# Kernel optimization log

Hardware: AMD Instinct MI355X
Metric: run time of the kernel (lower is better)

Reference implementation:

```python
import jax, jax.numpy as jnp
import numpy as np

N = 100000
E = 1600000
DIMS = [256, 192, 128, 64, 3]  # in_features=256, hidden_layer_count=4, last layer -> 3


def setup_inputs() -> dict:
    key = jax.random.key(0)
    ks = jax.random.split(key, 2 + 4 * len(DIMS))
    features = jax.random.normal(ks[0], (N, 256), dtype=jnp.float32)
    # (torch.unique-based normalization implicitly assumes this)
    src = jnp.arange(E, dtype=jnp.int64) % N
    dst = jax.random.randint(ks[1], (E,), 0, N, dtype=jnp.int64)
    edges = jnp.stack([src, dst], axis=1)
    inp = {"features": features, "edges": edges}
    ki = 2
    for li in range(4):
        din, dout = DIMS[li], DIMS[li + 1]
        s = 1.0 / np.sqrt(din)
        inp[f"W0_{li}"] = jax.random.uniform(ks[ki], (din, dout), jnp.float32, -s, s); ki += 1
        inp[f"b0_{li}"] = jax.random.uniform(ks[ki], (dout,), jnp.float32, -s, s); ki += 1
        inp[f"W1_{li}"] = jax.random.uniform(ks[ki], (din, dout), jnp.float32, -s, s); ki += 1
        inp[f"b1_{li}"] = jax.random.uniform(ks[ki], (dout,), jnp.float32, -s, s); ki += 1
    return inp


def _graph_conv_norm(x, edges, deg_inv, W0, b0, W1, b1):
    # pytorch3d GraphConv (undirected): w0(x) + scatter-add of w1(x[neighbor]) over both edge directions,
    # then degree normalization (GraphConvNorm)
    h0 = x @ W0 + b0                       # [N, dout]
    h1 = x @ W1 + b1                       # [N, dout]
    agg = jnp.zeros_like(h0)
    agg = agg.at[edges[:, 0]].add(h1[edges[:, 1]])
    agg = agg.at[edges[:, 1]].add(h1[edges[:, 0]])
    return deg_inv * (h0 + agg)


def reference(features, edges, W0_0, b0_0, W1_0, b1_0, W0_1, b0_1, W1_1, b1_1,
              W0_2, b0_2, W1_2, b1_2, W0_3, b0_3, W1_3, b1_3):
    # degree = occurrence count of each vertex id in edges (== torch.unique(..., return_counts=True)[1])
    deg = jnp.zeros((N,), jnp.float32).at[edges.reshape(-1)].add(1.0)
    deg_inv = (1.0 / deg)[:, None]
    params = [(W0_0, b0_0, W1_0, b1_0), (W0_1, b0_1, W1_1, b1_1), (W0_2, b0_2, W1_2, b1_2)]
    x = features
    for (W0, b0, W1, b1) in params:
        x = jax.nn.relu(_graph_conv_norm(x, edges, deg_inv, W0, b0, W1, b1))
    return _graph_conv_norm(x, edges, deg_inv, W0_3, b0_3, W1_3, b1_3)
```

## Files before the change

### kernel.cpp

```cpp
#include <hip/hip_runtime.h>
#include <hip/hip_fp16.h>

#define NV 100000
#define NE 1600000

#define BM 64
#define BN 64
#define BK 16

#define TBM 128
#define TBN 64
#define TBK 32
#define APAD 40
#define BPAD 40

#define SCAN_B 1024
#define NBLK ((NV + SCAN_B - 1) / SCAN_B)

typedef __attribute__((ext_vector_type(8))) _Float16 f16x8;
typedef __attribute__((ext_vector_type(4))) _Float16 f16x4;
typedef __attribute__((ext_vector_type(4))) float f32x4;

__global__ void degree_count(const int* __restrict__ ef, int* __restrict__ deg, int n) {
    int i = blockIdx.x * blockDim.x + threadIdx.x;
    if (i < n) atomicAdd(&deg[ef[i]], 1);
}

__global__ __launch_bounds__(SCAN_B) void scan_block(const int* __restrict__ deg,
                                                     int* __restrict__ part,
                                                     int* __restrict__ bsum, int n) {
    __shared__ int tmp[SCAN_B];
    const int tid = threadIdx.x;
    const int gid = blockIdx.x * SCAN_B + tid;
    int v = (gid < n) ? deg[gid] : 0;
    tmp[tid] = v;
    __syncthreads();
    for (int off = 1; off < SCAN_B; off <<= 1) {
        int t = (tid >= off) ? tmp[tid - off] : 0;
        __syncthreads();
        tmp[tid] += t;
        __syncthreads();
    }
    if (gid < n) part[gid] = tmp[tid] - v;
    if (tid == SCAN_B - 1) bsum[blockIdx.x] = tmp[tid];
}

__global__ __launch_bounds__(128) void scan_top(int* __restrict__ bsum, int nb) {
    __shared__ int tmp[128];
    const int tid = threadIdx.x;
    int v = (tid < nb) ? bsum[tid] : 0;
    tmp[tid] = v;
    __syncthreads();
    for (int off = 1; off < 128; off <<= 1) {
        int t = (tid >= off) ? tmp[tid - off] : 0;
        __syncthreads();
        tmp[tid] += t;
        __syncthreads();
    }
    if (tid < nb) bsum[tid] = tmp[tid] - v;
}

__global__ __launch_bounds__(SCAN_B) void finalize_rowptr(int* __restrict__ rowptr,
                                                          const int* __restrict__ bsum,
                                                          const int* __restrict__ deg,
                                                          int* __restrict__ fill,
                                                          float* __restrict__ dinv, int n) {
    const int gid = blockIdx.x * SCAN_B + threadIdx.x;
    if (gid < n) {
        int r = rowptr[gid] + bsum[blockIdx.x];
        rowptr[gid] = r;
        fill[gid] = r;
        dinv[gid] = 1.0f / (float)deg[gid];
    }
    if (gid == 0) rowptr[n] = 2 * NE;
}

__global__ void fill_adj(const int* __restrict__ edges, int* __restrict__ fill,
                         int* __restrict__ adj, int nE) {
    int e = blockIdx.x * blockDim.x + threadIdx.x;
    if (e >= nE) return;
    const int a = edges[2 * e];
    const int b = edges[2 * e + 1];
    int pa = atomicAdd(&fill[a], 1); adj[pa] = b;
    int pb = atomicAdd(&fill[b], 1); adj[pb] = a;
}

__global__ __launch_bounds__(256) void gemm_dual_mfma(
    const float* __restrict__ X,
    const float* __restrict__ W0, const float* __restrict__ b0,
    const float* __restrict__ W1, const float* __restrict__ b1,
    float* __restrict__ C0, _Float16* __restrict__ C1,
    int M, int din, int dout)
{
    __shared__ _Float16 As[TBM * APAD];
    __shared__ _Float16 Bs[2][TBN * BPAD];

    const int tid = threadIdx.x;
    const int bm = blockIdx.x * TBM;
    const int bn = blockIdx.y * TBN;
    const int lane = tid & 63;
    const int wid = tid >> 6;
    const int wm = wid >> 1;
    const int wn = wid & 1;
    const int lr = lane & 15;
    const int lk = lane >> 4;

    f32x4 acc[2][4][2] = {};

    const int bn_n = tid & 63;
    const int bn_kb = (tid >> 6) * 8;

    for (int k0 = 0; k0 < din; k0 += TBK) {
        #pragma unroll
        for (int i = 0; i < 4; ++i) {
            const int idx = tid + i * 256;
            const int row = idx >> 3;
            const int q = idx & 7;
            const int grow = bm + row;
            float4 v = {0.f, 0.f, 0.f, 0.f};
            if (grow < M)
                v = *reinterpret_cast<const float4*>(&X[(size_t)grow * din + k0 + q * 4]);
            f16x4 h = { (_Float16)v.x, (_Float16)v.y, (_Float16)v.z, (_Float16)v.w };
            *reinterpret_cast<f16x4*>(&As[row * APAD + q * 4]) = h;
        }
        {
            const float* pw0 = &W0[(size_t)(k0 + bn_kb) * dout + bn + bn_n];
            const float* pw1 = &W1[(size_t)(k0 + bn_kb) * dout + bn + bn_n];
            _Float16* d0 = &Bs[0][bn_n * BPAD + bn_kb];
            _Float16* d1 = &Bs[1][bn_n * BPAD + bn_kb];
            #pragma unroll
            for (int i = 0; i < 8; ++i) {
                d0[i] = (_Float16)pw0[(size_t)i * dout];
                d1[i] = (_Float16)pw1[(size_t)i * dout];
            }
        }
        __syncthreads();

        f16x8 a[4], b[2][2];
        #pragma unroll
        for (int mf = 0; mf < 4; ++mf)
            a[mf] = *reinterpret_cast<const f16x8*>(&As[(wm * 64 + mf * 16 + lr) * APAD + lk * 8]);
        #pragma unroll
        for (int o = 0; o < 2; ++o)
            #pragma unroll
            for (int nf = 0; nf < 2; ++nf)
                b[o][nf] = *reinterpret_cast<const f16x8*>(&Bs[o][(wn * 32 + nf * 16 + lr) * BPAD + lk * 8]);

        #pragma unroll
        for (int o = 0; o < 2; ++o)
            #pragma unroll
            for (int mf = 0; mf < 4; ++mf)
                #pragma unroll
                for (int nf = 0; nf < 2; ++nf)
                    acc[o][mf][nf] = __builtin_amdgcn_mfma_f32_16x16x32_f16(
                        a[mf], b[o][nf], acc[o][mf][nf], 0, 0, 0);

        __syncthreads();
    }

    #pragma unroll
    for (int mf = 0; mf < 4; ++mf) {
        #pragma unroll
        for (int reg = 0; reg < 4; ++reg) {
            const int row = bm + wm * 64 + mf * 16 + lk * 4 + reg;
            if (row >= M) continue;
            #pragma unroll
            for (int nf = 0; nf < 2; ++nf) {
                const int c = bn + wn * 32 + nf * 16 + lr;
                C0[(size_t)row * dout + c] = acc[0][mf][nf][reg] + b0[c];
                C1[(size_t)row * dout + c] = (_Float16)(acc[1][mf][nf][reg] + b1[c]);
            }
        }
    }
}

__global__ __launch_bounds__(256) void gemm_dual_bias_f32(
    const float* __restrict__ X,
    const float* __restrict__ W0, const float* __restrict__ b0,
    const float* __restrict__ W1, const float* __restrict__ b1,
    float* __restrict__ C0, float* __restrict__ C1,
    int M, int din, int dout)
{
    __shared__ float As[BM][BK + 1];
    __shared__ float Bs0[BK][BN];
    __shared__ float Bs1[BK][BN];

    const int tid = threadIdx.x;
    const int bm = blockIdx.x * BM;
    const int bn = blockIdx.y * BN;
    const int tx = tid & 15;
    const int ty = tid >> 4;

    const int ar = tid >> 2;
    const int ac = (tid & 3) * 4;
    const int br = tid >> 4;
    const int bc = (tid & 15) * 4;

    float acc0[4][4] = {};
    float acc1[4][4] = {};

    for (int k0 = 0; k0 < din; k0 += BK) {
        {
            const int grow = bm + ar;
            if (grow < M) {
                const float4 v = *reinterpret_cast<const float4*>(&X[(size_t)grow * din + k0 + ac]);
                As[ar][ac + 0] = v.x; As[ar][ac + 1] = v.y;
                As[ar][ac + 2] = v.z; As[ar][ac + 3] = v.w;
            } else {
                As[ar][ac + 0] = 0.f; As[ar][ac + 1] = 0.f;
                As[ar][ac + 2] = 0.f; As[ar][ac + 3] = 0.f;
            }
        }
        {
            const int gk = k0 + br;
            const int gc = bn + bc;
            float4 v0, v1;
            v0.x = (gc + 0 < dout) ? W0[(size_t)gk * dout + gc + 0] : 0.f;
            v0.y = (gc + 1 < dout) ? W0[(size_t)gk * dout + gc + 1] : 0.f;
            v0.z = (gc + 2 < dout) ? W0[(size_t)gk * dout + gc + 2] : 0.f;
            v0.w = (gc + 3 < dout) ? W0[(size_t)gk * dout + gc + 3] : 0.f;
            v1.x = (gc + 0 < dout) ? W1[(size_t)gk * dout + gc + 0] : 0.f;
            v1.y = (gc + 1 < dout) ? W1[(size_t)gk * dout + gc + 1] : 0.f;
            v1.z = (gc + 2 < dout) ? W1[(size_t)gk * dout + gc + 2] : 0.f;
            v1.w = (gc + 3 < dout) ? W1[(size_t)gk * dout + gc + 3] : 0.f;
            *reinterpret_cast<float4*>(&Bs0[br][bc]) = v0;
            *reinterpret_cast<float4*>(&Bs1[br][bc]) = v1;
        }
        __syncthreads();

        #pragma unroll
        for (int kk = 0; kk < BK; ++kk) {
            const float a0 = As[ty * 4 + 0][kk];
            const float a1 = As[ty * 4 + 1][kk];
            const float a2 = As[ty * 4 + 2][kk];
            const float a3 = As[ty * 4 + 3][kk];
            const float4 p = *reinterpret_cast<const float4*>(&Bs0[kk][tx * 4]);
            const float4 q = *reinterpret_cast<const float4*>(&Bs1[kk][tx * 4]);
            acc0[0][0] += a0 * p.x; acc0[0][1] += a0 * p.y; acc0[0][2] += a0 * p.z; acc0[0][3] += a0 * p.w;
            acc0[1][0] += a1 * p.x; acc0[1][1] += a1 * p.y; acc0[1][2] += a1 * p.z; acc0[1][3] += a1 * p.w;
            acc0[2][0] += a2 * p.x; acc0[2][1] += a2 * p.y; acc0[2][2] += a2 * p.z; acc0[2][3] += a2 * p.w;
            acc0[3][0] += a3 * p.x; acc0[3][1] += a3 * p.y; acc0[3][2] += a3 * p.z; acc0[3][3] += a3 * p.w;
            acc1[0][0] += a0 * q.x; acc1[0][1] += a0 * q.y; acc1[0][2] += a0 * q.z; acc1[0][3] += a0 * q.w;
            acc1[1][0] += a1 * q.x; acc1[1][1] += a1 * q.y; acc1[1][2] += a1 * q.z; acc1[1][3] += a1 * q.w;
            acc1[2][0] += a2 * q.x; acc1[2][1] += a2 * q.y; acc1[2][2] += a2 * q.z; acc1[2][3] += a2 * q.w;
            acc1[3][0] += a3 * q.x; acc1[3][1] += a3 * q.y; acc1[3][2] += a3 * q.z; acc1[3][3] += a3 * q.w;
        }
        __syncthreads();
    }

    #pragma unroll
    for (int i = 0; i < 4; ++i) {
        const int row = bm + ty * 4 + i;
        if (row >= M) continue;
        #pragma unroll
        for (int j = 0; j < 4; ++j) {
            const int col = bn + tx * 4 + j;
            if (col < dout) {
                C0[(size_t)row * dout + col] = acc0[i][j] + b0[col];
                C1[(size_t)row * dout + col] = acc1[i][j] + b1[col];
            }
        }
    }
}

__global__ __launch_bounds__(256) void gather_d192_h(
    const float* __restrict__ h0, const __half2* __restrict__ h1,
    const int* __restrict__ rowptr, const int* __restrict__ adj,
    const float* __restrict__ dinv, float* __restrict__ out)
{
    const int v = blockIdx.x * 4 + (threadIdx.x >> 6);
    if (v >= NV) return;
    const int lane = threadIdx.x & 63;
    const int sub = lane >> 5;
    const int cu = (lane & 31) * 3;
    const int s = rowptr[v], e = rowptr[v + 1];

    float2 a0 = {0.f, 0.f}, a1 = {0.f, 0.f}, a2 = {0.f, 0.f};

    int j = s;
    const int jend = s + ((e - s) & ~3);
    for (; j < jend; j += 4) {
        const __half2* r0 = h1 + (size_t)adj[j + sub] * 96 + cu;
        const __half2* r1 = h1 + (size_t)adj[j + 2 + sub] * 96 + cu;
        const float2 p0 = __half22float2(r0[0]);
        const float2 p1 = __half22float2(r0[1]);
        const float2 p2 = __half22float2(r0[2]);
        const float2 q0 = __half22float2(r1[0]);
        const float2 q1 = __half22float2(r1[1]);
        const float2 q2 = __half22float2(r1[2]);
        a0.x += p0.x + q0.x; a0.y += p0.y + q0.y;
        a1.x += p1.x + q1.x; a1.y += p1.y + q1.y;
        a2.x += p2.x + q2.x; a2.y += p2.y + q2.y;
    }
    for (; j < e; j += 2) {
        const int jj = j + sub;
        if (jj < e) {
            const __half2* r = h1 + (size_t)adj[jj] * 96 + cu;
            const float2 p0 = __half22float2(r[0]);
            const float2 p1 = __half22float2(r[1]);
            const float2 p2 = __half22float2(r[2]);
            a0.x += p0.x; a0.y += p0.y;
            a1.x += p1.x; a1.y += p1.y;
            a2.x += p2.x; a2.y += p2.y;
        }
    }

    a0.x += __shfl_xor(a0.x, 32); a0.y += __shfl_xor(a0.y, 32);
    a1.x += __shfl_xor(a1.x, 32); a1.y += __shfl_xor(a1.y, 32);
    a2.x += __shfl_xor(a2.x, 32); a2.y += __shfl_xor(a2.y, 32);

    if (sub == 0) {
        const float di = dinv[v];
        const size_t base = (size_t)v * 192 + (size_t)cu * 2;
        float2 o0, o1, o2;
        o0.x = fmaxf((h0[base + 0] + a0.x) * di, 0.f);
        o0.y = fmaxf((h0[base + 1] + a0.y) * di, 0.f);
        o1.x = fmaxf((h0[base + 2] + a1.x) * di, 0.f);
        o1.y = fmaxf((h0[base + 3] + a1.y) * di, 0.f);
        o2.x = fmaxf((h0[base + 4] + a2.x) * di, 0.f);
        o2.y = fmaxf((h0[base + 5] + a2.y) * di, 0.f);
        *reinterpret_cast<float2*>(out + base + 0) = o0;
        *reinterpret_cast<float2*>(out + base + 2) = o1;
        *reinterpret_cast<float2*>(out + base + 4) = o2;
    }
}

__global__ __launch_bounds__(256) void gather_d128_h(
    const float* __restrict__ h0, const __half2* __restrict__ h1,
    const int* __restrict__ rowptr, const int* __restrict__ adj,
    const float* __restrict__ dinv, float* __restrict__ out)
{
    const int v = blockIdx.x * 4 + (threadIdx.x >> 6);
    if (v >= NV) return;
    const int lane = threadIdx.x & 63;
    const int sub = lane >> 4;
    const int cu = (lane & 15) * 4;
    const int s = rowptr[v], e = rowptr[v + 1];

    float acc[8] = {};

    int j = s;
    const int jend = s + ((e - s) & ~7);
    for (; j < jend; j += 8) {
        const int4 w0 = *reinterpret_cast<const int4*>(h1 + (size_t)adj[j + sub] * 64 + cu);
        const int4 w1 = *reinterpret_cast<const int4*>(h1 + (size_t)adj[j + 4 + sub] * 64 + cu);
        #pragma unroll
        for (int t = 0; t < 4; ++t) {
            const float2 p = __half22float2(*(const __half2*)(&(&w0.x)[t]));
            const float2 q = __half22float2(*(const __half2*)(&(&w1.x)[t]));
            acc[2 * t + 0] += p.x + q.x;
            acc[2 * t + 1] += p.y + q.y;
        }
    }
    for (; j < e; j += 4) {
        const int jj = j + sub;
        if (jj < e) {
            const int4 w0 = *reinterpret_cast<const int4*>(h1 + (size_t)adj[jj] * 64 + cu);
            #pragma unroll
            for (int t = 0; t < 4; ++t) {
                const float2 p = __half22float2(*(const __half2*)(&(&w0.x)[t]));
                acc[2 * t + 0] += p.x;
                acc[2 * t + 1] += p.y;
            }
        }
    }

    #pragma unroll
    for (int t = 0; t < 8; ++t) {
        acc[t] += __shfl_xor(acc[t], 16);
        acc[t] += __shfl_xor(acc[t], 32);
    }

    if (sub == 0) {
        const float di = dinv[v];
        const size_t base = (size_t)v * 128 + (size_t)cu * 2;
        float4 o0, o1;
        o0.x = fmaxf((h0[base + 0] + acc[0]) * di, 0.f);
        o0.y = fmaxf((h0[base + 1] + acc[1]) * di, 0.f);
        o0.z = fmaxf((h0[base + 2] + acc[2]) * di, 0.f);
        o0.w = fmaxf((h0[base + 3] + acc[3]) * di, 0.f);
        o1.x = fmaxf((h0[base + 4] + acc[4]) * di, 0.f);
        o1.y = fmaxf((h0[base + 5] + acc[5]) * di, 0.f);
        o1.z = fmaxf((h0[base + 6] + acc[6]) * di, 0.f);
        o1.w = fmaxf((h0[base + 7] + acc[7]) * di, 0.f);
        *reinterpret_cast<float4*>(out + base + 0) = o0;
        *reinterpret_cast<float4*>(out + base + 4) = o1;
    }
}

__global__ __launch_bounds__(256) void gather_d64_h(
    const float* __restrict__ h0, const __half2* __restrict__ h1,
    const int* __restrict__ rowptr, const int* __restrict__ adj,
    const float* __restrict__ dinv, float* __restrict__ out)
{
    const int v = blockIdx.x * 4 + (threadIdx.x >> 6);
    if (v >= NV) return;
    const int lane = threadIdx.x & 63;
    const int sub = lane >> 3;
    const int cu = (lane & 7) * 4;
    const int s = rowptr[v], e = rowptr[v + 1];

    float acc[8] = {};

    int j = s;
    const int jend = s + ((e - s) & ~15);
    for (; j < jend; j += 16) {
        const int4 w0 = *reinterpret_cast<const int4*>(h1 + (size_t)adj[j + sub] * 32 + cu);
        const int4 w1 = *reinterpret_cast<const int4*>(h1 + (size_t)adj[j + 8 + sub] * 32 + cu);
        #pragma unroll
        for (int t = 0; t < 4; ++t) {
            const float2 p = __half22float2(*(const __half2*)(&(&w0.x)[t]));
            const float2 q = __half22float2(*(const __half2*)(&(&w1.x)[t]));
            acc[2 * t + 0] += p.x + q.x;
            acc[2 * t + 1] += p.y + q.y;
        }
    }
    for (; j < e; j += 8) {
        const int jj = j + sub;
        if (jj < e) {
            const int4 w0 = *reinterpret_cast<const int4*>(h1 + (size_t)adj[jj] * 32 + cu);
            #pragma unroll
            for (int t = 0; t < 4; ++t) {
                const float2 p = __half22float2(*(const __half2*)(&(&w0.x)[t]));
                acc[2 * t + 0] += p.x;
                acc[2 * t + 1] += p.y;
            }
        }
    }

    #pragma unroll
    for (int t = 0; t < 8; ++t) {
        acc[t] += __shfl_xor(acc[t], 8);
        acc[t] += __shfl_xor(acc[t], 16);
        acc[t] += __shfl_xor(acc[t], 32);
    }

    if (sub == 0) {
        const float di = dinv[v];
        const size_t base = (size_t)v * 64 + (size_t)cu * 2;
        float4 o0, o1;
        o0.x = fmaxf((h0[base + 0] + acc[0]) * di, 0.f);
        o0.y = fmaxf((h0[base + 1] + acc[1]) * di, 0.f);
        o0.z = fmaxf((h0[base + 2] + acc[2]) * di, 0.f);
        o0.w = fmaxf((h0[base + 3] + acc[3]) * di, 0.f);
        o1.x = fmaxf((h0[base + 4] + acc[4]) * di, 0.f);
        o1.y = fmaxf((h0[base + 5] + acc[5]) * di, 0.f);
        o1.z = fmaxf((h0[base + 6] + acc[6]) * di, 0.f);
        o1.w = fmaxf((h0[base + 7] + acc[7]) * di, 0.f);
        *reinterpret_cast<float4*>(out + base + 0) = o0;
        *reinterpret_cast<float4*>(out + base + 4) = o1;
    }
}

__global__ __launch_bounds__(256) void gather_d3(
    const float* __restrict__ h0, const float* __restrict__ h1,
    const int* __restrict__ rowptr, const int* __restrict__ adj,
    const float* __restrict__ dinv, float* __restrict__ out)
{
    const int v = blockIdx.x * 4 + (threadIdx.x >> 6);
    if (v >= NV) return;
    const int lane = threadIdx.x & 63;
    const int s = rowptr[v], e = rowptr[v + 1];
    float a0 = 0.f, a1 = 0.f, a2 = 0.f;
    for (int j = s + lane; j < e; j += 64) {
        const float3 r = *reinterpret_cast<const float3*>(h1 + (size_t)adj[j] * 3);
        a0 += r.x; a1 += r.y; a2 += r.z;
    }
    #pragma unroll
    for (int off = 1; off < 64; off <<= 1) {
        a0 += __shfl_xor(a0, off);
        a1 += __shfl_xor(a1, off);
        a2 += __shfl_xor(a2, off);
    }
    if (lane == 0) {
        const float di = dinv[v];
        const size_t base = (size_t)v * 3;
        out[base + 0] = (h0[base + 0] + a0) * di;
        out[base + 1] = (h0[base + 1] + a1) * di;
        out[base + 2] = (h0[base + 2] + a2) * di;
    }
}

extern "C" void kernel_launch(void* const* d_in, const int* in_sizes, int n_in,
                              void* d_out, int out_size, void* d_ws, size_t ws_size,
                              hipStream_t stream) {
    const float* features = (const float*)d_in[0];
    const int*   edges    = (const int*)d_in[1];

    char* ws = (char*)d_ws;
    size_t off = 0;
    auto alloc = [&](size_t bytes) {
        void* p = ws + off;
        off = (off + bytes + 255) & ~(size_t)255;
        return p;
    };
    int*   deg    = (int*)alloc((size_t)NV * sizeof(int));
    float* dinv   = (float*)alloc((size_t)NV * sizeof(float));
    int*   rowptr = (int*)alloc((size_t)(NV + 1) * sizeof(int));
    int*   fill   = (int*)alloc((size_t)NV * sizeof(int));
    int*   bsum   = (int*)alloc(256 * sizeof(int));
    int*   adj    = (int*)alloc((size_t)2 * NE * sizeof(int));
    float* buf0   = (float*)alloc((size_t)NV * 192 * sizeof(float));
    void*  buf1   = alloc((size_t)NV * 192 * sizeof(float));
    float* buf2   = (float*)alloc((size_t)NV * 128 * sizeof(float));

    hipMemsetAsync(deg, 0, (size_t)NV * sizeof(int), stream);
    degree_count<<<(2 * NE + 255) / 256, 256, 0, stream>>>(edges, deg, 2 * NE);
    scan_block<<<NBLK, SCAN_B, 0, stream>>>(deg, rowptr, bsum, NV);
    scan_top<<<1, 128, 0, stream>>>(bsum, NBLK);
    finalize_rowptr<<<NBLK, SCAN_B, 0, stream>>>(rowptr, bsum, deg, fill, dinv, NV);
    fill_adj<<<(NE + 255) / 256, 256, 0, stream>>>(edges, fill, adj, NE);

    const int dims[5] = {256, 192, 128, 64, 3};
    const float* Xp[4];
    float* C0p[4];
    Xp[0] = features; C0p[0] = buf0;
    Xp[1] = buf0;     C0p[1] = buf2;
    Xp[2] = buf2;     C0p[2] = buf0;
    Xp[3] = buf0;     C0p[3] = buf2;

    const int gatherGrid = (NV + 3) / 4;

    for (int li = 0; li < 4; ++li) {
        const int din  = dims[li];
        const int dout = dims[li + 1];
        const float* W0 = (const float*)d_in[2 + li * 4 + 0];
        const float* b0 = (const float*)d_in[2 + li * 4 + 1];
        const float* W1 = (const float*)d_in[2 + li * 4 + 2];
        const float* b1 = (const float*)d_in[2 + li * 4 + 3];

        if (li < 3) {
            dim3 grid((NV + TBM - 1) / TBM, dout / TBN);
            gemm_dual_mfma<<<grid, 256, 0, stream>>>(Xp[li], W0, b0, W1, b1,
                                                     C0p[li], (_Float16*)buf1, NV, din, dout);
        } else {
            dim3 grid((NV + BM - 1) / BM, (dout + BN - 1) / BN);
            gemm_dual_bias_f32<<<grid, 256, 0, stream>>>(Xp[li], W0, b0, W1, b1,
                                                         C0p[li], (float*)buf1, NV, din, dout);
        }

        float* dst = (li < 3) ? C0p[li] : (float*)d_out;
        if (li == 0)
            gather_d192_h<<<gatherGrid, 256, 0, stream>>>(C0p[li], (const __half2*)buf1,
                                                          rowptr, adj, dinv, dst);
        else if (li == 1)
            gather_d128_h<<<gatherGrid, 256, 0, stream>>>(C0p[li], (const __half2*)buf1,
                                                          rowptr, adj, dinv, dst);
        else if (li == 2)
            gather_d64_h<<<gatherGrid, 256, 0, stream>>>(C0p[li], (const __half2*)buf1,
                                                         rowptr, adj, dinv, dst);
        else
            gather_d3<<<gatherGrid, 256, 0, stream>>>(C0p[li], (const float*)buf1,
                                                      rowptr, adj, dinv, dst);
    }
}
```

Before: 806.5 us.

## Store inter-layer activations in fp16 and widen gather unrolling

The gather kernels now write ReLU activations as fp16 instead of fp32, and the following GEMMs read fp16 input directly through a templated load path. This halves activation write and read traffic between layers. The neighbor loops in the gather kernels are also unrolled to four rows per iteration for more memory-level parallelism, and the d64 gather is remapped to 16 lanes of 2 half2 each. The cost is reduced precision in the stored activations.

```diff
diff --git a/kernel.cpp b/kernel.cpp
--- a/kernel.cpp
+++ b/kernel.cpp
@@ -19,6 +19,7 @@
 
 typedef __attribute__((ext_vector_type(8))) _Float16 f16x8;
 typedef __attribute__((ext_vector_type(4))) _Float16 f16x4;
+typedef __attribute__((ext_vector_type(2))) _Float16 f16x2;
 typedef __attribute__((ext_vector_type(4))) float f32x4;
 
 __global__ void degree_count(const int* __restrict__ ef, int* __restrict__ deg, int n) {
@@ -85,8 +86,9 @@
     int pb = atomicAdd(&fill[b], 1); adj[pb] = a;
 }
 
+template <typename XT>
 __global__ __launch_bounds__(256) void gemm_dual_mfma(
-    const float* __restrict__ X,
+    const XT* __restrict__ X,
     const float* __restrict__ W0, const float* __restrict__ b0,
     const float* __restrict__ W1, const float* __restrict__ b1,
     float* __restrict__ C0, _Float16* __restrict__ C1,
@@ -111,17 +113,31 @@
     const int bn_kb = (tid >> 6) * 8;
 
     for (int k0 = 0; k0 < din; k0 += TBK) {
-        #pragma unroll
-        for (int i = 0; i < 4; ++i) {
-            const int idx = tid + i * 256;
-            const int row = idx >> 3;
-            const int q = idx & 7;
-            const int grow = bm + row;
-            float4 v = {0.f, 0.f, 0.f, 0.f};
-            if (grow < M)
-                v = *reinterpret_cast<const float4*>(&X[(size_t)grow * din + k0 + q * 4]);
-            f16x4 h = { (_Float16)v.x, (_Float16)v.y, (_Float16)v.z, (_Float16)v.w };
-            *reinterpret_cast<f16x4*>(&As[row * APAD + q * 4]) = h;
+        if constexpr (sizeof(XT) == 4) {
+            #pragma unroll
+            for (int i = 0; i < 4; ++i) {
+                const int idx = tid + i * 256;
+                const int row = idx >> 3;
+                const int q = idx & 7;
+                const int grow = bm + row;
+                float4 v = {0.f, 0.f, 0.f, 0.f};
+                if (grow < M)
+                    v = *reinterpret_cast<const float4*>(&X[(size_t)grow * din + k0 + q * 4]);
+                f16x4 h = { (_Float16)v.x, (_Float16)v.y, (_Float16)v.z, (_Float16)v.w };
+                *reinterpret_cast<f16x4*>(&As[row * APAD + q * 4]) = h;
+            }
+        } else {
+            #pragma unroll
+            for (int i = 0; i < 2; ++i) {
+                const int idx = tid + i * 256;
+                const int row = idx >> 2;
+                const int q = idx & 3;
+                const int grow = bm + row;
+                f16x8 h = {};
+                if (grow < M)
+                    h = *reinterpret_cast<const f16x8*>(&X[(size_t)grow * din + k0 + q * 8]);
+                *reinterpret_cast<f16x8*>(&As[row * APAD + q * 8]) = h;
+            }
         }
         {
             const float* pw0 = &W0[(size_t)(k0 + bn_kb) * dout + bn + bn_n];
@@ -175,7 +191,7 @@
 }
 
 __global__ __launch_bounds__(256) void gemm_dual_bias_f32(
-    const float* __restrict__ X,
+    const _Float16* __restrict__ X,
     const float* __restrict__ W0, const float* __restrict__ b0,
     const float* __restrict__ W1, const float* __restrict__ b1,
     float* __restrict__ C0, float* __restrict__ C1,
@@ -203,9 +219,9 @@
         {
             const int grow = bm + ar;
             if (grow < M) {
-                const float4 v = *reinterpret_cast<const float4*>(&X[(size_t)grow * din + k0 + ac]);
-                As[ar][ac + 0] = v.x; As[ar][ac + 1] = v.y;
-                As[ar][ac + 2] = v.z; As[ar][ac + 3] = v.w;
+                const f16x4 v = *reinterpret_cast<const f16x4*>(&X[(size_t)grow * din + k0 + ac]);
+                As[ar][ac + 0] = (float)v[0]; As[ar][ac + 1] = (float)v[1];
+                As[ar][ac + 2] = (float)v[2]; As[ar][ac + 3] = (float)v[3];
             } else {
                 As[ar][ac + 0] = 0.f; As[ar][ac + 1] = 0.f;
                 As[ar][ac + 2] = 0.f; As[ar][ac + 3] = 0.f;
@@ -266,7 +282,7 @@
 __global__ __launch_bounds__(256) void gather_d192_h(
     const float* __restrict__ h0, const __half2* __restrict__ h1,
     const int* __restrict__ rowptr, const int* __restrict__ adj,
-    const float* __restrict__ dinv, float* __restrict__ out)
+    const float* __restrict__ dinv, _Float16* __restrict__ out)
 {
     const int v = blockIdx.x * 4 + (threadIdx.x >> 6);
     if (v >= NV) return;
@@ -278,30 +294,42 @@
     float2 a0 = {0.f, 0.f}, a1 = {0.f, 0.f}, a2 = {0.f, 0.f};
 
     int j = s;
-    const int jend = s + ((e - s) & ~3);
-    for (; j < jend; j += 4) {
-        const __half2* r0 = h1 + (size_t)adj[j + sub] * 96 + cu;
-        const __half2* r1 = h1 + (size_t)adj[j + 2 + sub] * 96 + cu;
-        const float2 p0 = __half22float2(r0[0]);
-        const float2 p1 = __half22float2(r0[1]);
-        const float2 p2 = __half22float2(r0[2]);
-        const float2 q0 = __half22float2(r1[0]);
-        const float2 q1 = __half22float2(r1[1]);
-        const float2 q2 = __half22float2(r1[2]);
-        a0.x += p0.x + q0.x; a0.y += p0.y + q0.y;
-        a1.x += p1.x + q1.x; a1.y += p1.y + q1.y;
-        a2.x += p2.x + q2.x; a2.y += p2.y + q2.y;
+    const int jend = s + ((e - s) & ~7);
+    for (; j < jend; j += 8) {
+        const int u0 = adj[j + 0 + sub];
+        const int u1 = adj[j + 2 + sub];
+        const int u2 = adj[j + 4 + sub];
+        const int u3 = adj[j + 6 + sub];
+        const __half2* r0 = h1 + (size_t)u0 * 96 + cu;
+        const __half2* r1 = h1 + (size_t)u1 * 96 + cu;
+        const __half2* r2 = h1 + (size_t)u2 * 96 + cu;
+        const __half2* r3 = h1 + (size_t)u3 * 96 + cu;
+        const __half2 x00 = r0[0], x01 = r0[1], x02 = r0[2];
+        const __half2 x10 = r1[0], x11 = r1[1], x12 = r1[2];
+        const __half2 x20 = r2[0], x21 = r2[1], x22 = r2[2];
+        const __half2 x30 = r3[0], x31 = r3[1], x32 = r3[2];
+        float2 p;
+        p = __half22float2(x00); a0.x += p.x; a0.y += p.y;
+        p = __half22float2(x01); a1.x += p.x; a1.y += p.y;
+        p = __half22float2(x02); a2.x += p.x; a2.y += p.y;
+        p = __half22float2(x10); a0.x += p.x; a0.y += p.y;
+        p = __half22float2(x11); a1.x += p.x; a1.y += p.y;
+        p = __half22float2(x12); a2.x += p.x; a2.y += p.y;
+        p = __half22float2(x20); a0.x += p.x; a0.y += p.y;
+        p = __half22float2(x21); a1.x += p.x; a1.y += p.y;
+        p = __half22float2(x22); a2.x += p.x; a2.y += p.y;
+        p = __half22float2(x30); a0.x += p.x; a0.y += p.y;
+        p = __half22float2(x31); a1.x += p.x; a1.y += p.y;
+        p = __half22float2(x32); a2.x += p.x; a2.y += p.y;
     }
     for (; j < e; j += 2) {
         const int jj = j + sub;
         if (jj < e) {
             const __half2* r = h1 + (size_t)adj[jj] * 96 + cu;
-            const float2 p0 = __half22float2(r[0]);
-            const float2 p1 = __half22float2(r[1]);
-            const float2 p2 = __half22float2(r[2]);
-            a0.x += p0.x; a0.y += p0.y;
-            a1.x += p1.x; a1.y += p1.y;
-            a2.x += p2.x; a2.y += p2.y;
+            float2 p;
+            p = __half22float2(r[0]); a0.x += p.x; a0.y += p.y;
+            p = __half22float2(r[1]); a1.x += p.x; a1.y += p.y;
+            p = __half22float2(r[2]); a2.x += p.x; a2.y += p.y;
         }
     }
 
@@ -312,23 +340,23 @@
     if (sub == 0) {
         const float di = dinv[v];
         const size_t base = (size_t)v * 192 + (size_t)cu * 2;
-        float2 o0, o1, o2;
-        o0.x = fmaxf((h0[base + 0] + a0.x) * di, 0.f);
-        o0.y = fmaxf((h0[base + 1] + a0.y) * di, 0.f);
-        o1.x = fmaxf((h0[base + 2] + a1.x) * di, 0.f);
-        o1.y = fmaxf((h0[base + 3] + a1.y) * di, 0.f);
-        o2.x = fmaxf((h0[base + 4] + a2.x) * di, 0.f);
-        o2.y = fmaxf((h0[base + 5] + a2.y) * di, 0.f);
-        *reinterpret_cast<float2*>(out + base + 0) = o0;
-        *reinterpret_cast<float2*>(out + base + 2) = o1;
-        *reinterpret_cast<float2*>(out + base + 4) = o2;
+        f16x2 o0, o1, o2;
+        o0[0] = (_Float16)fmaxf((h0[base + 0] + a0.x) * di, 0.f);
+        o0[1] = (_Float16)fmaxf((h0[base + 1] + a0.y) * di, 0.f);
+        o1[0] = (_Float16)fmaxf((h0[base + 2] + a1.x) * di, 0.f);
+        o1[1] = (_Float16)fmaxf((h0[base + 3] + a1.y) * di, 0.f);
+        o2[0] = (_Float16)fmaxf((h0[base + 4] + a2.x) * di, 0.f);
+        o2[1] = (_Float16)fmaxf((h0[base + 5] + a2.y) * di, 0.f);
+        *reinterpret_cast<f16x2*>(out + base + 0) = o0;
+        *reinterpret_cast<f16x2*>(out + base + 2) = o1;
+        *reinterpret_cast<f16x2*>(out + base + 4) = o2;
     }
 }
 
 __global__ __launch_bounds__(256) void gather_d128_h(
     const float* __restrict__ h0, const __half2* __restrict__ h1,
     const int* __restrict__ rowptr, const int* __restrict__ adj,
-    const float* __restrict__ dinv, float* __restrict__ out)
+    const float* __restrict__ dinv, _Float16* __restrict__ out)
 {
     const int v = blockIdx.x * 4 + (threadIdx.x >> 6);
     if (v >= NV) return;
@@ -340,16 +368,24 @@
     float acc[8] = {};
 
     int j = s;
-    const int jend = s + ((e - s) & ~7);
-    for (; j < jend; j += 8) {
-        const int4 w0 = *reinterpret_cast<const int4*>(h1 + (size_t)adj[j + sub] * 64 + cu);
-        const int4 w1 = *reinterpret_cast<const int4*>(h1 + (size_t)adj[j + 4 + sub] * 64 + cu);
+    const int jend = s + ((e - s) & ~15);
+    for (; j < jend; j += 16) {
+        const int u0 = adj[j + 0 + sub];
+        const int u1 = adj[j + 4 + sub];
+        const int u2 = adj[j + 8 + sub];
+        const int u3 = adj[j + 12 + sub];
+        const int4 w0 = *reinterpret_cast<const int4*>(h1 + (size_t)u0 * 64 + cu);
+        const int4 w1 = *reinterpret_cast<const int4*>(h1 + (size_t)u1 * 64 + cu);
+        const int4 w2 = *reinterpret_cast<const int4*>(h1 + (size_t)u2 * 64 + cu);
+        const int4 w3 = *reinterpret_cast<const int4*>(h1 + (size_t)u3 * 64 + cu);
         #pragma unroll
         for (int t = 0; t < 4; ++t) {
-            const float2 p = __half22float2(*(const __half2*)(&(&w0.x)[t]));
-            const float2 q = __half22float2(*(const __half2*)(&(&w1.x)[t]));
-            acc[2 * t + 0] += p.x + q.x;
-            acc[2 * t + 1] += p.y + q.y;
+            const float2 p0 = __half22float2(*(const __half2*)(&(&w0.x)[t]));
+            const float2 p1 = __half22float2(*(const __half2*)(&(&w1.x)[t]));
+            const float2 p2 = __half22float2(*(const __half2*)(&(&w2.x)[t]));
+            const float2 p3 = __half22float2(*(const __half2*)(&(&w3.x)[t]));
+            acc[2 * t + 0] += (p0.x + p1.x) + (p2.x + p3.x);
+            acc[2 * t + 1] += (p0.y + p1.y) + (p2.y + p3.y);
         }
     }
     for (; j < e; j += 4) {
@@ -374,53 +410,55 @@
     if (sub == 0) {
         const float di = dinv[v];
         const size_t base = (size_t)v * 128 + (size_t)cu * 2;
-        float4 o0, o1;
-        o0.x = fmaxf((h0[base + 0] + acc[0]) * di, 0.f);
-        o0.y = fmaxf((h0[base + 1] + acc[1]) * di, 0.f);
-        o0.z = fmaxf((h0[base + 2] + acc[2]) * di, 0.f);
-        o0.w = fmaxf((h0[base + 3] + acc[3]) * di, 0.f);
-        o1.x = fmaxf((h0[base + 4] + acc[4]) * di, 0.f);
-        o1.y = fmaxf((h0[base + 5] + acc[5]) * di, 0.f);
-        o1.z = fmaxf((h0[base + 6] + acc[6]) * di, 0.f);
-        o1.w = fmaxf((h0[base + 7] + acc[7]) * di, 0.f);
-        *reinterpret_cast<float4*>(out + base + 0) = o0;
-        *reinterpret_cast<float4*>(out + base + 4) = o1;
+        f16x8 o;
+        #pragma unroll
+        for (int t = 0; t < 8; ++t)
+            o[t] = (_Float16)fmaxf((h0[base + t] + acc[t]) * di, 0.f);
+        *reinterpret_cast<f16x8*>(out + base) = o;
     }
 }
 
 __global__ __launch_bounds__(256) void gather_d64_h(
     const float* __restrict__ h0, const __half2* __restrict__ h1,
     const int* __restrict__ rowptr, const int* __restrict__ adj,
-    const float* __restrict__ dinv, float* __restrict__ out)
+    const float* __restrict__ dinv, _Float16* __restrict__ out)
 {
     const int v = blockIdx.x * 4 + (threadIdx.x >> 6);
     if (v >= NV) return;
     const int lane = threadIdx.x & 63;
-    const int sub = lane >> 3;
-    const int cu = (lane & 7) * 4;
+    const int sub = lane >> 4;
+    const int cu = (lane & 15) * 2;
     const int s = rowptr[v], e = rowptr[v + 1];
 
-    float acc[8] = {};
+    float acc[4] = {};
 
     int j = s;
     const int jend = s + ((e - s) & ~15);
     for (; j < jend; j += 16) {
-        const int4 w0 = *reinterpret_cast<const int4*>(h1 + (size_t)adj[j + sub] * 32 + cu);
-        const int4 w1 = *reinterpret_cast<const int4*>(h1 + (size_t)adj[j + 8 + sub] * 32 + cu);
-        #pragma unroll
-        for (int t = 0; t < 4; ++t) {
-            const float2 p = __half22float2(*(const __half2*)(&(&w0.x)[t]));
-            const float2 q = __half22float2(*(const __half2*)(&(&w1.x)[t]));
-            acc[2 * t + 0] += p.x + q.x;
-            acc[2 * t + 1] += p.y + q.y;
-        }
-    }
-    for (; j < e; j += 8) {
+        const int u0 = adj[j + 0 + sub];
+        const int u1 = adj[j + 4 + sub];
+        const int u2 = adj[j + 8 + sub];
+        const int u3 = adj[j + 12 + sub];
+        const int2 w0 = *reinterpret_cast<const int2*>(h1 + (size_t)u0 * 32 + cu);
+        const int2 w1 = *reinterpret_cast<const int2*>(h1 + (size_t)u1 * 32 + cu);
+        const int2 w2 = *reinterpret_cast<const int2*>(h1 + (size_t)u2 * 32 + cu);
+        const int2 w3 = *reinterpret_cast<const int2*>(h1 + (size_t)u3 * 32 + cu);
+        #pragma unroll
+        for (int t = 0; t < 2; ++t) {
+            const float2 p0 = __half22float2(*(const __half2*)(&(&w0.x)[t]));
+            const float2 p1 = __half22float2(*(const __half2*)(&(&w1.x)[t]));
+            const float2 p2 = __half22float2(*(const __half2*)(&(&w2.x)[t]));
+            const float2 p3 = __half22float2(*(const __half2*)(&(&w3.x)[t]));
+            acc[2 * t + 0] += (p0.x + p1.x) + (p2.x + p3.x);
+            acc[2 * t + 1] += (p0.y + p1.y) + (p2.y + p3.y);
+        }
+    }
+    for (; j < e; j += 4) {
         const int jj = j + sub;
         if (jj < e) {
-            const int4 w0 = *reinterpret_cast<const int4*>(h1 + (size_t)adj[jj] * 32 + cu);
-            #pragma unroll
-            for (int t = 0; t < 4; ++t) {
+            const int2 w0 = *reinterpret_cast<const int2*>(h1 + (size_t)adj[jj] * 32 + cu);
+            #pragma unroll
+            for (int t = 0; t < 2; ++t) {
                 const float2 p = __half22float2(*(const __half2*)(&(&w0.x)[t]));
                 acc[2 * t + 0] += p.x;
                 acc[2 * t + 1] += p.y;
@@ -429,8 +467,7 @@
     }
 
     #pragma unroll
-    for (int t = 0; t < 8; ++t) {
-        acc[t] += __shfl_xor(acc[t], 8);
+    for (int t = 0; t < 4; ++t) {
         acc[t] += __shfl_xor(acc[t], 16);
         acc[t] += __shfl_xor(acc[t], 32);
     }
@@ -438,17 +475,11 @@
     if (sub == 0) {
         const float di = dinv[v];
         const size_t base = (size_t)v * 64 + (size_t)cu * 2;
-        float4 o0, o1;
-        o0.x = fmaxf((h0[base + 0] + acc[0]) * di, 0.f);
-        o0.y = fmaxf((h0[base + 1] + acc[1]) * di, 0.f);
-        o0.z = fmaxf((h0[base + 2] + acc[2]) * di, 0.f);
-        o0.w = fmaxf((h0[base + 3] + acc[3]) * di, 0.f);
-        o1.x = fmaxf((h0[base + 4] + acc[4]) * di, 0.f);
-        o1.y = fmaxf((h0[base + 5] + acc[5]) * di, 0.f);
-        o1.z = fmaxf((h0[base + 6] + acc[6]) * di, 0.f);
-        o1.w = fmaxf((h0[base + 7] + acc[7]) * di, 0.f);
-        *reinterpret_cast<float4*>(out + base + 0) = o0;
-        *reinterpret_cast<float4*>(out + base + 4) = o1;
+        f16x4 o;
+        #pragma unroll
+        for (int t = 0; t < 4; ++t)
+            o[t] = (_Float16)fmaxf((h0[base + t] + acc[t]) * di, 0.f);
+        *reinterpret_cast<f16x4*>(out + base) = o;
     }
 }
 
@@ -494,15 +525,16 @@
         off = (off + bytes + 255) & ~(size_t)255;
         return p;
     };
-    int*   deg    = (int*)alloc((size_t)NV * sizeof(int));
-    float* dinv   = (float*)alloc((size_t)NV * sizeof(float));
-    int*   rowptr = (int*)alloc((size_t)(NV + 1) * sizeof(int));
-    int*   fill   = (int*)alloc((size_t)NV * sizeof(int));
-    int*   bsum   = (int*)alloc(256 * sizeof(int));
-    int*   adj    = (int*)alloc((size_t)2 * NE * sizeof(int));
-    float* buf0   = (float*)alloc((size_t)NV * 192 * sizeof(float));
-    void*  buf1   = alloc((size_t)NV * 192 * sizeof(float));
-    float* buf2   = (float*)alloc((size_t)NV * 128 * sizeof(float));
+    int*      deg    = (int*)alloc((size_t)NV * sizeof(int));
+    float*    dinv   = (float*)alloc((size_t)NV * sizeof(float));
+    int*      rowptr = (int*)alloc((size_t)(NV + 1) * sizeof(int));
+    int*      fill   = (int*)alloc((size_t)NV * sizeof(int));
+    int*      bsum   = (int*)alloc(256 * sizeof(int));
+    int*      adj    = (int*)alloc((size_t)2 * NE * sizeof(int));
+    float*    bufC0  = (float*)alloc((size_t)NV * 192 * sizeof(float));
+    void*     bufC1  = alloc((size_t)NV * 192 * sizeof(float));
+    _Float16* bufX1  = (_Float16*)alloc((size_t)NV * 192 * sizeof(_Float16));
+    _Float16* bufX2  = (_Float16*)alloc((size_t)NV * 128 * sizeof(_Float16));
 
     hipMemsetAsync(deg, 0, (size_t)NV * sizeof(int), stream);
     degree_count<<<(2 * NE + 255) / 256, 256, 0, stream>>>(edges, deg, 2 * NE);
@@ -511,15 +543,10 @@
     finalize_rowptr<<<NBLK, SCAN_B, 0, stream>>>(rowptr, bsum, deg, fill, dinv, NV);
     fill_adj<<<(NE + 255) / 256, 256, 0, stream>>>(edges, fill, adj, NE);
 
+    const int gatherGrid = (NV + 3) / 4;
     const int dims[5] = {256, 192, 128, 64, 3};
-    const float* Xp[4];
-    float* C0p[4];
-    Xp[0] = features; C0p[0] = buf0;
-    Xp[1] = buf0;     C0p[1] = buf2;
-    Xp[2] = buf2;     C0p[2] = buf0;
-    Xp[3] = buf0;     C0p[3] = buf2;
-
-    const int gatherGrid = (NV + 3) / 4;
+    _Float16* Xh[4] = { nullptr, bufX1, bufX2, bufX1 };
+    _Float16* Xout[3] = { bufX1, bufX2, bufX1 };
 
     for (int li = 0; li < 4; ++li) {
         const int din  = dims[li];
@@ -529,28 +556,31 @@
         const float* W1 = (const float*)d_in[2 + li * 4 + 2];
         const float* b1 = (const float*)d_in[2 + li * 4 + 3];
 
-        if (li < 3) {
+        if (li == 0) {
             dim3 grid((NV + TBM - 1) / TBM, dout / TBN);
-            gemm_dual_mfma<<<grid, 256, 0, stream>>>(Xp[li], W0, b0, W1, b1,
-                                                     C0p[li], (_Float16*)buf1, NV, din, dout);
+            gemm_dual_mfma<float><<<grid, 256, 0, stream>>>(features, W0, b0, W1, b1,
+                                                            bufC0, (_Float16*)bufC1, NV, din, dout);
+        } else if (li < 3) {
+            dim3 grid((NV + TBM - 1) / TBM, dout / TBN);
+            gemm_dual_mfma<_Float16><<<grid, 256, 0, stream>>>(Xh[li], W0, b0, W1, b1,
+                                                               bufC0, (_Float16*)bufC1, NV, din, dout);
         } else {
             dim3 grid((NV + BM - 1) / BM, (dout + BN - 1) / BN);
-            gemm_dual_bias_f32<<<grid, 256, 0, stream>>>(Xp[li], W0, b0, W1, b1,
-                                                         C0p[li], (float*)buf1, NV, din, dout);
-        }
-
-        float* dst = (li < 3) ? C0p[li] : (float*)d_out;
+            gemm_dual_bias_f32<<<grid, 256, 0, stream>>>(Xh[li], W0, b0, W1, b1,
+                                                         bufC0, (float*)bufC1, NV, din, dout);
+        }
+
         if (li == 0)
-            gather_d192_h<<<gatherGrid, 256, 0, stream>>>(C0p[li], (const __half2*)buf1,
-                                                          rowptr, adj, dinv, dst);
+            gather_d192_h<<<gatherGrid, 256, 0, stream>>>(bufC0, (const __half2*)bufC1,
+                                                          rowptr, adj, dinv, Xout[0]);
         else if (li == 1)
-            gather_d128_h<<<gatherGrid, 256, 0, stream>>>(C0p[li], (const __half2*)buf1,
-                                                          rowptr, adj, dinv, dst);
+            gather_d128_h<<<gatherGrid, 256, 0, stream>>>(bufC0, (const __half2*)bufC1,
+                                                          rowptr, adj, dinv, Xout[1]);
         else if (li == 2)
-            gather_d64_h<<<gatherGrid, 256, 0, stream>>>(C0p[li], (const __half2*)buf1,
-                                                         rowptr, adj, dinv, dst);
+            gather_d64_h<<<gatherGrid, 256, 0, stream>>>(bufC0, (const __half2*)bufC1,
+                                                         rowptr, adj, dinv, Xout[2]);
         else
-            gather_d3<<<gatherGrid, 256, 0, stream>>>(C0p[li], (const float*)buf1,
-                                                      rowptr, adj, dinv, dst);
-    }
-}
+            gather_d3<<<gatherGrid, 256, 0, stream>>>(bufC0, (const float*)bufC1,
+                                                      rowptr, adj, dinv, (float*)d_out);
+    }
+}
```

After: 786.2 us. 2.5% less time.
